# Performance work log

Measured on AMD Instinct MI355X. Metric: run time of the kernel, lower is better.

## Reference

```python
import jax, jax.numpy as jnp
import numpy as np

DIM = 192
HEADS = 6
WS = 7          # window size
SHIFT = 3       # shift size
HID = 768       # mlp hidden
EPS = 1e-5


def _rel_pos_index(ws):
    coords = np.stack(np.meshgrid(np.arange(ws), np.arange(ws), indexing='ij'))  # (2, ws, ws)
    cf = coords.reshape(2, -1)                       # (2, ws*ws)
    rel = cf[:, :, None] - cf[:, None, :]            # (2, N, N)
    rel = rel.transpose(1, 2, 0).astype(np.int64)
    rel[:, :, 0] += ws - 1
    rel[:, :, 1] += ws - 1
    rel[:, :, 0] *= 2 * ws - 1
    return jnp.asarray(rel.sum(-1))                  # (N, N)

REL_IDX = _rel_pos_index(WS)


def _layernorm(x, w, b):
    mu = jnp.mean(x, axis=-1, keepdims=True)
    var = jnp.mean(jnp.square(x - mu), axis=-1, keepdims=True)
    return (x - mu) * jax.lax.rsqrt(var + EPS) * w + b


def setup_inputs() -> dict:
    key = jax.random.key(0)
    ks = jax.random.split(key, 8)
    B, H, W = 32, 56, 56
    s = 0.02
    return {
        'x': jax.random.normal(ks[0], (B, H * W, DIM), jnp.float32),
        'norm1_w': jnp.ones((DIM,), jnp.float32),
        'norm1_b': jnp.zeros((DIM,), jnp.float32),
        'qkv_w': jax.random.normal(ks[1], (3 * DIM, DIM), jnp.float32) * s,
        'qkv_b': jnp.zeros((3 * DIM,), jnp.float32),
        'rpb_table': jax.random.normal(ks[2], ((2 * WS - 1) ** 2, HEADS), jnp.float32) * s,
        'proj_w': jax.random.normal(ks[3], (DIM, DIM), jnp.float32) * s,
        'proj_b': jnp.zeros((DIM,), jnp.float32),
        'norm2_w': jnp.ones((DIM,), jnp.float32),
        'norm2_b': jnp.zeros((DIM,), jnp.float32),
        'fc1_w': jax.random.normal(ks[4], (HID, DIM), jnp.float32) * s,
        'fc1_b': jnp.zeros((HID,), jnp.float32),
        'fc2_w': jax.random.normal(ks[5], (DIM, HID), jnp.float32) * s,
        'fc2_b': jnp.zeros((DIM,), jnp.float32),
        'H': H,
        'W': W,
    }


def reference(x, norm1_w, norm1_b, qkv_w, qkv_b, rpb_table, proj_w, proj_b,
              norm2_w, norm2_b, fc1_w, fc1_b, fc2_w, fc2_b, H, W):
    B, L, C = x.shape
    d = C // HEADS
    scale = d ** -0.5
    N = WS * WS

    shortcut = x
    h = _layernorm(x, norm1_w, norm1_b).reshape(B, H, W, C)
    if SHIFT > 0:
        h = jnp.roll(h, shift=(-SHIFT, -SHIFT), axis=(1, 2))

    # window partition -> (B * nW, N, C)
    h = h.reshape(B, H // WS, WS, W // WS, WS, C).transpose(0, 1, 3, 2, 4, 5)
    hw = h.reshape(-1, N, C)

    # windowed attention (NOTE: the torch block never passes a shift mask)
    qkv = hw @ qkv_w.T + qkv_b                                    # (B_, N, 3C)
    qkv = qkv.reshape(-1, N, 3, HEADS, d).transpose(2, 0, 3, 1, 4)
    q, k, v = qkv[0] * scale, qkv[1], qkv[2]                      # (B_, h, N, d)
    attn = jnp.einsum('bhnd,bhmd->bhnm', q, k)
    bias = rpb_table[REL_IDX].transpose(2, 0, 1)                  # (h, N, N)
    attn = jax.nn.softmax(attn + bias[None], axis=-1)
    out = jnp.einsum('bhnm,bhmd->bhnd', attn, v)
    out = out.transpose(0, 2, 1, 3).reshape(-1, N, C)
    out = out @ proj_w.T + proj_b

    # window reverse -> (B, H, W, C)
    out = out.reshape(B, H // WS, W // WS, WS, WS, C).transpose(0, 1, 3, 2, 4, 5)
    out = out.reshape(B, H, W, C)
    if SHIFT > 0:
        out = jnp.roll(out, shift=(SHIFT, SHIFT), axis=(1, 2))

    x = shortcut + out.reshape(B, L, C)
    h2 = _layernorm(x, norm2_w, norm2_b)
    mlp = jax.nn.gelu(h2 @ fc1_w.T + fc1_b, approximate=False) @ fc2_w.T + fc2_b
    return x + mlp
```

## Files before the change

### kernel.cpp

```cpp
#include <hip/hip_runtime.h>
#include <hip/hip_bf16.h>
#include <cmath>

typedef float f32x4 __attribute__((ext_vector_type(4)));
typedef __bf16 bf16x8 __attribute__((ext_vector_type(8)));
typedef __bf16 bf16x4 __attribute__((ext_vector_type(4)));

#define WS_SZ 7
#define SHIFT 3
#define HGRID 56
#define C_DIM 192
#define NHEADS 6
#define HDIM 32
#define NTOK 100352
#define NWIN 2048

__device__ __forceinline__ int win_to_tok(int wrow) {
    int w = wrow / 49, i = wrow - w * 49;
    int b = w >> 6, rem = w & 63;
    int wy = rem >> 3, wx = rem & 7;
    int yi = i / 7, xi = i - yi * 7;
    int y = wy * 7 + yi + SHIFT; if (y >= HGRID) y -= HGRID;
    int x = wx * 7 + xi + SHIFT; if (x >= HGRID) x -= HGRID;
    return b * (HGRID * HGRID) + y * HGRID + x;
}

__global__ __launch_bounds__(256)
void cvt_kernel(const float* __restrict__ src, __bf16* __restrict__ dst, int n8)
{
    int idx = blockIdx.x * 256 + threadIdx.x;
    if (idx >= n8) return;
    float4 a = ((const float4*)src)[idx * 2];
    float4 b = ((const float4*)src)[idx * 2 + 1];
    bf16x8 o;
    o[0] = (__bf16)a.x; o[1] = (__bf16)a.y; o[2] = (__bf16)a.z; o[3] = (__bf16)a.w;
    o[4] = (__bf16)b.x; o[5] = (__bf16)b.y; o[6] = (__bf16)b.z; o[7] = (__bf16)b.w;
    ((bf16x8*)dst)[idx] = o;
}

__global__ __launch_bounds__(256)
void bias_expand_kernel(const float* __restrict__ rpb, float* __restrict__ bias_g)
{
    int idx = blockIdx.x * 256 + threadIdx.x;
    if (idx >= NHEADS * 2401) return;
    int h = idx / 2401, rem = idx - h * 2401;
    int i = rem / 49, j = rem - i * 49;
    int yi = i / 7, xi = i - yi * 7;
    int yj = j / 7, xj = j - yj * 7;
    int ri = (yi - yj + 6) * 13 + (xi - xj + 6);
    bias_g[idx] = rpb[ri * NHEADS + h];
}

template<int WINDOWED>
__global__ __launch_bounds__(256)
void ln_kernel(const float* __restrict__ x, const float* __restrict__ w,
               const float* __restrict__ b, __bf16* __restrict__ out)
{
    int r = blockIdx.x * 4 + (threadIdx.x >> 6);
    int lane = threadIdx.x & 63;
    int src = WINDOWED ? win_to_tok(r) : r;
    const float* xp = x + (size_t)src * C_DIM;
    float v0 = xp[lane], v1 = xp[lane + 64], v2 = xp[lane + 128];
    float s = v0 + v1 + v2;
    float sq = v0 * v0 + v1 * v1 + v2 * v2;
    #pragma unroll
    for (int off = 32; off; off >>= 1) {
        s  += __shfl_xor(s, off);
        sq += __shfl_xor(sq, off);
    }
    float mu = s * (1.f / C_DIM);
    float rs = rsqrtf(sq * (1.f / C_DIM) - mu * mu + 1e-5f);
    __bf16* op = out + (size_t)r * C_DIM;
    op[lane]       = (__bf16)((v0 - mu) * rs * w[lane]       + b[lane]);
    op[lane + 64]  = (__bf16)((v1 - mu) * rs * w[lane + 64]  + b[lane + 64]);
    op[lane + 128] = (__bf16)((v2 - mu) * rs * w[lane + 128] + b[lane + 128]);
}

template<int MODE>
__global__ __launch_bounds__(256)
void gemm_kernel(const __bf16* __restrict__ A, const __bf16* __restrict__ W,
                 const float* __restrict__ bias, void* __restrict__ outp,
                 const float* __restrict__ resid, int N, int K)
{
    __shared__ __bf16 As[128 * 40];
    __shared__ __bf16 Bs[64 * 40];
    const int tid = threadIdx.x;
    const int wave = tid >> 6, lane = tid & 63;
    const int wm = wave >> 1, wn = wave & 1;
    const int l15 = lane & 15, q8 = (lane >> 4) << 3;
    const int m0 = blockIdx.y * 128, n0 = blockIdx.x * 64;

    f32x4 acc[4][2];
    f32x4 zero = {0.f, 0.f, 0.f, 0.f};
    #pragma unroll
    for (int i = 0; i < 4; i++)
        #pragma unroll
        for (int j = 0; j < 2; j++) acc[i][j] = zero;

    const int br = tid >> 2, bc = (tid & 3) << 3;
    for (int kt = 0; kt < K; kt += 32) {
        __syncthreads();
        #pragma unroll
        for (int it = 0; it < 2; it++) {
            int idx = it * 256 + tid;
            int r = idx >> 2, c = (idx & 3) << 3;
            *(uint4*)(&As[r * 40 + c]) =
                *(const uint4*)(A + (size_t)(m0 + r) * K + kt + c);
        }
        *(uint4*)(&Bs[br * 40 + bc]) =
            *(const uint4*)(W + (size_t)(n0 + br) * K + kt + bc);
        __syncthreads();
        bf16x8 af[4], bfr[2];
        #pragma unroll
        for (int fm = 0; fm < 4; fm++)
            af[fm] = *(const bf16x8*)(&As[(wm * 64 + fm * 16 + l15) * 40 + q8]);
        #pragma unroll
        for (int fn = 0; fn < 2; fn++)
            bfr[fn] = *(const bf16x8*)(&Bs[(wn * 32 + fn * 16 + l15) * 40 + q8]);
        #pragma unroll
        for (int fm = 0; fm < 4; fm++)
            #pragma unroll
            for (int fn = 0; fn < 2; fn++)
                acc[fm][fn] = __builtin_amdgcn_mfma_f32_16x16x32_bf16(
                    af[fm], bfr[fn], acc[fm][fn], 0, 0, 0);
    }

    const int l4 = lane >> 4;
    #pragma unroll
    for (int fm = 0; fm < 4; fm++) {
        #pragma unroll
        for (int fn = 0; fn < 2; fn++) {
            int c = n0 + wn * 32 + fn * 16 + l15;
            float bv = bias[c];
            #pragma unroll
            for (int r = 0; r < 4; r++) {
                int m = m0 + wm * 64 + fm * 16 + l4 * 4 + r;
                float v = acc[fm][fn][r] + bv;
                if (MODE == 0) {
                    ((__bf16*)outp)[(size_t)m * N + c] = (__bf16)v;
                } else {
                    int t = win_to_tok(m);
                    ((float*)outp)[(size_t)t * C_DIM + c] =
                        resid[(size_t)t * C_DIM + c] + v;
                }
            }
        }
    }
}

__global__ __launch_bounds__(256, 3)
void mlp_fused_kernel(const float* __restrict__ n2w, const float* __restrict__ n2b,
                      const __bf16* __restrict__ w1,
                      const float* __restrict__ b1,
                      const __bf16* __restrict__ w2,
                      const float* __restrict__ b2,
                      float* __restrict__ out)
{
    __shared__ __align__(16) __bf16 As[64 * 200];
    __shared__ __bf16 Hs[64 * 72];
    const int tid = threadIdx.x;
    const int wn = tid >> 6, lane = tid & 63;
    const int l15 = lane & 15, q4 = lane >> 4, q8 = q4 << 3;
    const int m0 = blockIdx.x * 64;
    const int r0 = wn * 16;

    const __bf16* w1base = w1 + (size_t)(wn * 16 + l15) * 192 + q8;
    const __bf16* w2base = w2 + (size_t)(wn * 48 + l15) * 768 + q8;

    f32x4 zero = {0.f, 0.f, 0.f, 0.f};

    bf16x8 w1f[2][6];
    #pragma unroll
    for (int kt = 0; kt < 6; ++kt)
        w1f[0][kt] = *(const bf16x8*)(w1base + kt * 32);

    float bv1s[12];
    #pragma unroll
    for (int ch = 0; ch < 12; ++ch)
        bv1s[ch] = b1[ch * 64 + wn * 16 + l15];
    float bv2s[3];
    #pragma unroll
    for (int tn = 0; tn < 3; ++tn)
        bv2s[tn] = b2[wn * 48 + tn * 16 + l15];

    {
        const float wl0 = n2w[lane], wl1 = n2w[lane + 64], wl2 = n2w[lane + 128];
        const float bl0 = n2b[lane], bl1 = n2b[lane + 64], bl2 = n2b[lane + 128];
        #pragma unroll
        for (int rr = 0; rr < 16; ++rr) {
            const float* xp = out + (size_t)(m0 + r0 + rr) * C_DIM;
            float v0 = xp[lane], v1 = xp[lane + 64], v2 = xp[lane + 128];
            float s = v0 + v1 + v2;
            float sq = v0 * v0 + v1 * v1 + v2 * v2;
            #pragma unroll
            for (int off = 32; off; off >>= 1) {
                s  += __shfl_xor(s, off);
                sq += __shfl_xor(sq, off);
            }
            float mu = s * (1.f / C_DIM);
            float rs = rsqrtf(sq * (1.f / C_DIM) - mu * mu + 1e-5f);
            As[(r0 + rr) * 200 + lane]       = (__bf16)((v0 - mu) * rs * wl0 + bl0);
            As[(r0 + rr) * 200 + lane + 64]  = (__bf16)((v1 - mu) * rs * wl1 + bl1);
            As[(r0 + rr) * 200 + lane + 128] = (__bf16)((v2 - mu) * rs * wl2 + bl2);
        }
    }
    __syncthreads();

    f32x4 acc2[4][3];
    #pragma unroll
    for (int tm = 0; tm < 4; ++tm)
        #pragma unroll
        for (int tn = 0; tn < 3; ++tn) acc2[tm][tn] = zero;

    bf16x8 w2f[6];

    #pragma unroll
    for (int ch = 0; ch < 12; ++ch) {
        const int h0 = ch * 64;
        const int cur = ch & 1, nxt = cur ^ 1;

        if (ch < 11) {
            #pragma unroll
            for (int kt = 0; kt < 6; ++kt)
                w1f[nxt][kt] = *(const bf16x8*)(w1base + (size_t)(h0 + 64) * 192 + kt * 32);
        }
        #pragma unroll
        for (int ks = 0; ks < 2; ++ks)
            #pragma unroll
            for (int tn = 0; tn < 3; ++tn)
                w2f[ks * 3 + tn] = *(const bf16x8*)(w2base + (size_t)(tn * 16) * 768 + h0 + ks * 32);

        f32x4 acc1[4];
        #pragma unroll
        for (int tm = 0; tm < 4; ++tm) acc1[tm] = zero;
        #pragma unroll
        for (int kt = 0; kt < 6; ++kt)
            #pragma unroll
            for (int tm = 0; tm < 4; ++tm) {
                bf16x8 af = *(const bf16x8*)(&As[(tm * 16 + l15) * 200 + kt * 32 + q8]);
                acc1[tm] = __builtin_amdgcn_mfma_f32_16x16x32_bf16(
                    af, w1f[cur][kt], acc1[tm], 0, 0, 0);
            }

        __syncthreads();

        {
            const float bv = bv1s[ch];
            #pragma unroll
            for (int tm = 0; tm < 4; ++tm)
                #pragma unroll
                for (int r = 0; r < 4; ++r) {
                    int row = tm * 16 + q4 * 4 + r;
                    float v = acc1[tm][r] + bv;
                    float g = v * __builtin_amdgcn_rcpf(1.f + __expf(-1.702f * v));
                    Hs[row * 72 + wn * 16 + l15] = (__bf16)g;
                }
        }
        __syncthreads();

        #pragma unroll
        for (int ks = 0; ks < 2; ++ks)
            #pragma unroll
            for (int tm = 0; tm < 4; ++tm) {
                bf16x8 ap = *(const bf16x8*)(&Hs[(tm * 16 + l15) * 72 + ks * 32 + q8]);
                #pragma unroll
                for (int tn = 0; tn < 3; ++tn)
                    acc2[tm][tn] = __builtin_amdgcn_mfma_f32_16x16x32_bf16(
                        ap, w2f[ks * 3 + tn], acc2[tm][tn], 0, 0, 0);
            }
    }

    float* Cs = (float*)As;
    #pragma unroll
    for (int pass = 0; pass < 2; ++pass) {
        if (pass) __syncthreads();
        #pragma unroll
        for (int tmh = 0; tmh < 2; ++tmh) {
            int tm = pass * 2 + tmh;
            #pragma unroll
            for (int tn = 0; tn < 3; ++tn) {
                int c = wn * 48 + tn * 16 + l15;
                float bv = bv2s[tn];
                #pragma unroll
                for (int r = 0; r < 4; ++r) {
                    int rl = tmh * 16 + q4 * 4 + r;
                    Cs[rl * 196 + c] = acc2[tm][tn][r] + bv;
                }
            }
        }
        __syncthreads();
        #pragma unroll
        for (int it = 0; it < 6; ++it) {
            int f = it * 256 + tid;
            int row = f / 48, c4 = f - row * 48;
            float4* gp = (float4*)(out + (size_t)(m0 + pass * 32 + row) * C_DIM) + c4;
            float4 g = *gp;
            const float* lp = &Cs[row * 196 + c4 * 4];
            g.x += lp[0]; g.y += lp[1]; g.z += lp[2]; g.w += lp[3];
            *gp = g;
        }
    }
}

__global__ __launch_bounds__(256, 2)
void attn_mfma_kernel(const __bf16* __restrict__ qkv,
                      const float* __restrict__ bias_g,
                      __bf16* __restrict__ out)
{
    const int wave = threadIdx.x >> 6;
    const int lane = threadIdx.x & 63;
    const int pair = blockIdx.x * 4 + wave;
    const int w = pair / 6, head = pair - (pair / 6) * 6;

    __shared__ __bf16 vsT_s[4][32 * 72];
    __shared__ __bf16 Ps_s[4][64 * 72];
    __bf16* vsT = vsT_s[wave];
    __bf16* Ps  = Ps_s[wave];

    const int l15 = lane & 15, q4 = lane >> 4, q8 = q4 << 3;
    const size_t qbase = (size_t)w * 49 * 576 + head * 32;

    {
        int d = lane & 31, jh = lane >> 5;
        #pragma unroll
        for (int it = 0; it < 25; ++it) {
            int j = it * 2 + jh;
            if (j < 49)
                vsT[d * 72 + j] = qkv[qbase + (size_t)j * 576 + 384 + d];
        }
        for (int idx = lane; idx < 32 * 15; idx += 64) {
            int dd = idx / 15, jj = 49 + (idx - dd * 15);
            vsT[dd * 72 + jj] = (__bf16)0.f;
        }
    }

    bf16x8 qf[4], kf[4];
    #pragma unroll
    for (int t = 0; t < 4; ++t) {
        int row = t * 16 + l15;
        int rq = row < 49 ? row : 48;
        qf[t] = *(const bf16x8*)(qkv + qbase + (size_t)rq * 576 + q8);
        kf[t] = *(const bf16x8*)(qkv + qbase + (size_t)rq * 576 + 192 + q8);
    }

    f32x4 sc[4][4];
    f32x4 zero = {0.f, 0.f, 0.f, 0.f};
    #pragma unroll
    for (int tn = 0; tn < 4; ++tn)
        #pragma unroll
        for (int tm = 0; tm < 4; ++tm) sc[tn][tm] = zero;
    __builtin_amdgcn_s_setprio(1);
    #pragma unroll
    for (int tn = 0; tn < 4; ++tn)
        #pragma unroll
        for (int tm = 0; tm < 4; ++tm)
            sc[tn][tm] = __builtin_amdgcn_mfma_f32_16x16x32_bf16(
                kf[tn], qf[tm], sc[tn][tm], 0, 0, 0);
    __builtin_amdgcn_s_setprio(0);

    const float scale = 0.17677669529663687f;
    const int hbase = head * 2401;
    const int jb4 = q4 * 4;
    #pragma unroll
    for (int tm = 0; tm < 4; ++tm) {
        int i = tm * 16 + l15;
        int ioff = hbase + (i < 49 ? i : 48) * 49;
        float v[4][4];
        #pragma unroll
        for (int tn = 0; tn < 4; ++tn) {
            int jb = tn * 16 + jb4;
            #pragma unroll
            for (int r = 0; r < 4; ++r) {
                int j = jb + r;
                float bz = (j < 49) ? bias_g[ioff + j] : 0.f;
                float t = sc[tn][tm][r] * scale + bz;
                v[tn][r] = (j < 49) ? t : -1e30f;
            }
        }
        float mx = v[0][0];
        #pragma unroll
        for (int tn = 0; tn < 4; ++tn)
            #pragma unroll
            for (int r = 0; r < 4; ++r) mx = fmaxf(mx, v[tn][r]);
        mx = fmaxf(mx, __shfl_xor(mx, 16));
        mx = fmaxf(mx, __shfl_xor(mx, 32));
        float sm = 0.f;
        #pragma unroll
        for (int tn = 0; tn < 4; ++tn)
            #pragma unroll
            for (int r = 0; r < 4; ++r) {
                float e = __expf(v[tn][r] - mx);
                v[tn][r] = e;
                sm += e;
            }
        sm += __shfl_xor(sm, 16);
        sm += __shfl_xor(sm, 32);
        float inv = __builtin_amdgcn_rcpf(sm);
        if (i < 49) {
            #pragma unroll
            for (int tn = 0; tn < 4; ++tn) {
                int jb = tn * 16 + jb4;
                bf16x4 pk;
                #pragma unroll
                for (int r = 0; r < 4; ++r)
                    pk[r] = (__bf16)((jb + r < 49) ? v[tn][r] * inv : 0.f);
                *(bf16x4*)(&Ps[i * 72 + jb]) = pk;
            }
        }
    }


    f32x4 oc[4][2];
    #pragma unroll
    for (int tm = 0; tm < 4; ++tm)
        #pragma unroll
        for (int tn = 0; tn < 2; ++tn) oc[tm][tn] = zero;
    #pragma unroll
    for (int ks = 0; ks < 2; ++ks) {
        bf16x8 bv[2];
        #pragma unroll
        for (int tn = 0; tn < 2; ++tn)
            bv[tn] = *(const bf16x8*)(vsT + (tn * 16 + l15) * 72 + ks * 32 + q8);
        __builtin_amdgcn_s_setprio(1);
        #pragma unroll
        for (int tm = 0; tm < 4; ++tm) {
            bf16x8 ap = *(const bf16x8*)(Ps + (tm * 16 + l15) * 72 + ks * 32 + q8);
            #pragma unroll
            for (int tn = 0; tn < 2; ++tn)
                oc[tm][tn] = __builtin_amdgcn_mfma_f32_16x16x32_bf16(
                    ap, bv[tn], oc[tm][tn], 0, 0, 0);
        }
        __builtin_amdgcn_s_setprio(0);
    }

    #pragma unroll
    for (int tm = 0; tm < 4; ++tm) {
        #pragma unroll
        for (int r = 0; r < 4; ++r) {
            int m = tm * 16 + q4 * 4 + r;
            if (m < 49) {
                __bf16* op = out + (size_t)(w * 49 + m) * C_DIM + head * 32;
                #pragma unroll
                for (int tn = 0; tn < 2; ++tn)
                    op[tn * 16 + l15] = (__bf16)(oc[tm][tn][r]);
            }
        }
    }
}

extern "C" void kernel_launch(void* const* d_in, const int* in_sizes, int n_in,
                              void* d_out, int out_size, void* d_ws, size_t ws_size,
                              hipStream_t stream) {
    const float* x     = (const float*)d_in[0];
    const float* n1w   = (const float*)d_in[1];
    const float* n1b   = (const float*)d_in[2];
    const float* qkvw  = (const float*)d_in[3];
    const float* qkvb  = (const float*)d_in[4];
    const float* rpb   = (const float*)d_in[5];
    const float* projw = (const float*)d_in[6];
    const float* projb = (const float*)d_in[7];
    const float* n2w   = (const float*)d_in[8];
    const float* n2b   = (const float*)d_in[9];
    const float* fc1w  = (const float*)d_in[10];
    const float* fc1b  = (const float*)d_in[11];
    const float* fc2w  = (const float*)d_in[12];
    const float* fc2b  = (const float*)d_in[13];
    float* out = (float*)d_out;
    char* ws = (char*)d_ws;

    __bf16* bufA    = (__bf16*)ws;
    __bf16* bufQ    = (__bf16*)(ws + 38535168);
    __bf16* qkvw_b  = (__bf16*)(ws + 154140672);
    __bf16* projw_b = (__bf16*)(ws + 154361856);
    __bf16* fc1w_b  = (__bf16*)(ws + 154435584);
    __bf16* fc2w_b  = (__bf16*)(ws + 154730496);
    float*  bias_g  = (float*) (ws + 155025408);

    cvt_kernel<<<(110592/8 + 255)/256, 256, 0, stream>>>(qkvw, qkvw_b, 110592/8);
    cvt_kernel<<<(36864/8  + 255)/256, 256, 0, stream>>>(projw, projw_b, 36864/8);
    cvt_kernel<<<(147456/8 + 255)/256, 256, 0, stream>>>(fc1w, fc1w_b, 147456/8);
    cvt_kernel<<<(147456/8 + 255)/256, 256, 0, stream>>>(fc2w, fc2w_b, 147456/8);
    bias_expand_kernel<<<(NHEADS*2401 + 255)/256, 256, 0, stream>>>(rpb, bias_g);

    ln_kernel<1><<<NTOK / 4, 256, 0, stream>>>(x, n1w, n1b, bufA);
    gemm_kernel<0><<<dim3(9, NTOK / 128), 256, 0, stream>>>(
        bufA, qkvw_b, qkvb, bufQ, nullptr, 576, 192);
    attn_mfma_kernel<<<NWIN * NHEADS / 4, 256, 0, stream>>>(bufQ, bias_g, bufA);
    gemm_kernel<1><<<dim3(3, NTOK / 128), 256, 0, stream>>>(
        bufA, projw_b, projb, (void*)out, x, 192, 192);
    mlp_fused_kernel<<<NTOK / 64, 256, 0, stream>>>(
        n2w, n2b, fc1w_b, fc1b, fc2w_b, fc2b, out);
}
```

Before: 464.1 us.

## Fuse LayerNorm1 with QKV projection GEMM into one kernel

Replaces the separate LN kernel and QKV GEMM with a single kernel in which each block normalizes 128 windowed rows into shared memory, then each wave computes all 576 output columns for its 32 rows using MFMA, streaming weight fragments from global memory with double buffering. This removes the round trip of the normalized activation through global memory and one kernel launch. In exchange, each wave reads the whole QKV weight matrix from global or L2 with no shared-memory reuse across waves. Output stores are scattered 2-byte writes, and grid parallelism drops to 784 blocks.

```diff
diff --git a/kernel.cpp b/kernel.cpp
--- a/kernel.cpp
+++ b/kernel.cpp
@@ -51,29 +51,88 @@
     bias_g[idx] = rpb[ri * NHEADS + h];
 }
 
-template<int WINDOWED>
-__global__ __launch_bounds__(256)
-void ln_kernel(const float* __restrict__ x, const float* __restrict__ w,
-               const float* __restrict__ b, __bf16* __restrict__ out)
+__global__ __launch_bounds__(256, 3)
+void qkv_ln_kernel(const float* __restrict__ x, const float* __restrict__ n1w,
+                   const float* __restrict__ n1b,
+                   const __bf16* __restrict__ qw,
+                   const float* __restrict__ qb,
+                   __bf16* __restrict__ outq)
 {
-    int r = blockIdx.x * 4 + (threadIdx.x >> 6);
-    int lane = threadIdx.x & 63;
-    int src = WINDOWED ? win_to_tok(r) : r;
-    const float* xp = x + (size_t)src * C_DIM;
-    float v0 = xp[lane], v1 = xp[lane + 64], v2 = xp[lane + 128];
-    float s = v0 + v1 + v2;
-    float sq = v0 * v0 + v1 * v1 + v2 * v2;
-    #pragma unroll
-    for (int off = 32; off; off >>= 1) {
-        s  += __shfl_xor(s, off);
-        sq += __shfl_xor(sq, off);
-    }
-    float mu = s * (1.f / C_DIM);
-    float rs = rsqrtf(sq * (1.f / C_DIM) - mu * mu + 1e-5f);
-    __bf16* op = out + (size_t)r * C_DIM;
-    op[lane]       = (__bf16)((v0 - mu) * rs * w[lane]       + b[lane]);
-    op[lane + 64]  = (__bf16)((v1 - mu) * rs * w[lane + 64]  + b[lane + 64]);
-    op[lane + 128] = (__bf16)((v2 - mu) * rs * w[lane + 128] + b[lane + 128]);
+    __shared__ __bf16 As[128 * 200];
+    const int tid = threadIdx.x;
+    const int wn = tid >> 6, lane = tid & 63;
+    const int l15 = lane & 15, q4 = lane >> 4, q8 = q4 << 3;
+    const int m0 = blockIdx.x * 128;
+    const int r0 = wn * 32;
+    __bf16* As_w = &As[r0 * 200];
+
+    bf16x8 wf[2][6];
+    #pragma unroll
+    for (int kt = 0; kt < 6; ++kt)
+        wf[0][kt] = *(const bf16x8*)(qw + (size_t)l15 * 192 + kt * 32 + q8);
+    float bvf[2];
+    bvf[0] = qb[l15];
+
+    {
+        const float wl0 = n1w[lane], wl1 = n1w[lane + 64], wl2 = n1w[lane + 128];
+        const float bl0 = n1b[lane], bl1 = n1b[lane + 64], bl2 = n1b[lane + 128];
+        #pragma unroll 4
+        for (int rr = 0; rr < 32; ++rr) {
+            const float* xp = x + (size_t)win_to_tok(m0 + r0 + rr) * C_DIM;
+            float v0 = xp[lane], v1 = xp[lane + 64], v2 = xp[lane + 128];
+            float s = v0 + v1 + v2;
+            float sq = v0 * v0 + v1 * v1 + v2 * v2;
+            #pragma unroll
+            for (int off = 32; off; off >>= 1) {
+                s  += __shfl_xor(s, off);
+                sq += __shfl_xor(sq, off);
+            }
+            float mu = s * (1.f / C_DIM);
+            float rs = rsqrtf(sq * (1.f / C_DIM) - mu * mu + 1e-5f);
+            As_w[rr * 200 + lane]       = (__bf16)((v0 - mu) * rs * wl0 + bl0);
+            As_w[rr * 200 + lane + 64]  = (__bf16)((v1 - mu) * rs * wl1 + bl1);
+            As_w[rr * 200 + lane + 128] = (__bf16)((v2 - mu) * rs * wl2 + bl2);
+        }
+    }
+
+    bf16x8 af[6][2];
+    #pragma unroll
+    for (int kt = 0; kt < 6; ++kt)
+        #pragma unroll
+        for (int tm = 0; tm < 2; ++tm)
+            af[kt][tm] = *(const bf16x8*)(&As_w[(tm * 16 + l15) * 200 + kt * 32 + q8]);
+
+    f32x4 zero = {0.f, 0.f, 0.f, 0.f};
+
+    #pragma unroll 4
+    for (int tn = 0; tn < 36; ++tn) {
+        const int cur = tn & 1, nxt = cur ^ 1;
+        if (tn < 35) {
+            #pragma unroll
+            for (int kt = 0; kt < 6; ++kt)
+                wf[nxt][kt] = *(const bf16x8*)(qw + (size_t)((tn + 1) * 16 + l15) * 192 + kt * 32 + q8);
+            bvf[nxt] = qb[(tn + 1) * 16 + l15];
+        }
+        f32x4 acc[2];
+        acc[0] = zero; acc[1] = zero;
+        __builtin_amdgcn_s_setprio(1);
+        #pragma unroll
+        for (int kt = 0; kt < 6; ++kt)
+            #pragma unroll
+            for (int tm = 0; tm < 2; ++tm)
+                acc[tm] = __builtin_amdgcn_mfma_f32_16x16x32_bf16(
+                    af[kt][tm], wf[cur][kt], acc[tm], 0, 0, 0);
+        __builtin_amdgcn_s_setprio(0);
+        const float bv = bvf[cur];
+        const int c = tn * 16 + l15;
+        #pragma unroll
+        for (int tm = 0; tm < 2; ++tm)
+            #pragma unroll
+            for (int r = 0; r < 4; ++r) {
+                int m = m0 + r0 + tm * 16 + q4 * 4 + r;
+                outq[(size_t)m * 576 + c] = (__bf16)(acc[tm][r] + bv);
+            }
+    }
 }
 
 template<int MODE>
@@ -482,9 +541,8 @@
     cvt_kernel<<<(147456/8 + 255)/256, 256, 0, stream>>>(fc2w, fc2w_b, 147456/8);
     bias_expand_kernel<<<(NHEADS*2401 + 255)/256, 256, 0, stream>>>(rpb, bias_g);
 
-    ln_kernel<1><<<NTOK / 4, 256, 0, stream>>>(x, n1w, n1b, bufA);
-    gemm_kernel<0><<<dim3(9, NTOK / 128), 256, 0, stream>>>(
-        bufA, qkvw_b, qkvb, bufQ, nullptr, 576, 192);
+    qkv_ln_kernel<<<NTOK / 128, 256, 0, stream>>>(
+        x, n1w, n1b, qkvw_b, qkvb, bufQ);
     attn_mfma_kernel<<<NWIN * NHEADS / 4, 256, 0, stream>>>(bufQ, bias_g, bufA);
     gemm_kernel<1><<<dim3(3, NTOK / 128), 256, 0, stream>>>(
         bufA, projw_b, projb, (void*)out, x, 192, 192);
```

New measurement: 527.8 us. 1.14x slower.
